# Kernel optimization log

Measured on AMD Instinct MI355X. Metric: run time of the kernel, lower is better.

The kernel has to match this reference:

```python
import jax, jax.numpy as jnp
import numpy as np

B, S, T, D = 4, 2, 1024, 512
H = 8
HD = D // H
EPS = 1e-6
LN_EPS = 1e-5


def setup_inputs() -> dict:
    key = jax.random.key(0)
    ks = jax.random.split(key, 12)
    def lin(k, fan_in, shape):
        bound = 1.0 / np.sqrt(fan_in)
        return jax.random.uniform(k, shape, jnp.float32, -bound, bound)
    return {
        "hidden_states": jax.random.normal(ks[0], (B, S, T, D), jnp.float32),
        "Wq": lin(ks[1], D, (D, D)), "bq": lin(ks[2], D, (D,)),
        "Wk": lin(ks[3], D, (D, D)), "bk": lin(ks[4], D, (D,)),
        "Wv": lin(ks[5], D, (D, D)), "bv": lin(ks[6], D, (D,)),
        "Wo": lin(ks[7], D, (D, D)), "bo": lin(ks[8], D, (D,)),
        "ln_g": jnp.ones((S, D), jnp.float32),
        "ln_b": jnp.zeros((S, D), jnp.float32),
        "gate_alpha": jnp.full((S,), 0.01, jnp.float32),
    }


def _heads(x):
    # [B,T,D] -> [B,H,T,HD]
    return x.reshape(B, T, H, HD).transpose(0, 2, 1, 3)


def _layernorm(x, g, b):
    mu = jnp.mean(x, axis=-1, keepdims=True)
    var = jnp.var(x, axis=-1, keepdims=True)
    return (x - mu) * jax.lax.rsqrt(var + LN_EPS) * g + b


def reference(hidden_states, Wq, bq, Wk, bk, Wv, bv, Wo, bo, ln_g, ln_b, gate_alpha):
    h1, h2 = hidden_states[:, 0], hidden_states[:, 1]  # [B,T,D]
    proj = lambda x, W, b: jnp.einsum('btd,ed->bte', x, W) + b
    Q1, K1, V1 = _heads(proj(h1, Wq, bq)), _heads(proj(h1, Wk, bk)), _heads(proj(h1, Wv, bv))
    Q2, K2, V2 = _heads(proj(h2, Wq, bq)), _heads(proj(h2, Wk, bk)), _heads(proj(h2, Wv, bv))
    scale = 1.0 / np.sqrt(HD)
    L12 = jnp.einsum('bhqd,bhkd->bhqk', Q1, K2) * scale
    L21 = jnp.einsum('bhqd,bhkd->bhqk', Q2, K1) * scale
    S12 = jax.nn.softmax(L12, axis=-1)
    S21 = jax.nn.softmax(L21, axis=-1)
    M = S12 + S21 + EPS
    A12 = S12 / M
    A21 = S21 / M
    H1 = jnp.einsum('bhqk,bhkd->bhqd', A12, V2).transpose(0, 2, 1, 3).reshape(B, T, D)
    H2 = jnp.einsum('bhqk,bhkd->bhqd', A21, V1).transpose(0, 2, 1, 3).reshape(B, T, D)
    H1 = _layernorm(jnp.einsum('btd,ed->bte', H1, Wo) + bo, ln_g[0], ln_b[0])
    H2 = _layernorm(jnp.einsum('btd,ed->bte', H2, Wo) + bo, ln_g[1], ln_b[1])
    attn = jnp.stack([H1, H2], axis=1)  # [B,2,T,D]
    return hidden_states + attn * gate_alpha[None, :, None, None]
```

## Files before the change

### kernel.cpp

```cpp
#include <hip/hip_runtime.h>

#define DEVI __device__ __forceinline__

typedef __bf16 v8bf __attribute__((ext_vector_type(8)));
typedef float  v4f  __attribute__((ext_vector_type(4)));
typedef short  v4s  __attribute__((ext_vector_type(4)));

DEVI unsigned short f2bf(float f) {
  unsigned u = __builtin_bit_cast(unsigned, f);
  u += 0x7fffu + ((u >> 16) & 1u);
  return (unsigned short)(u >> 16);
}
DEVI v4f MFMA32(v8bf a, v8bf b, v4f c) {
  return __builtin_amdgcn_mfma_f32_16x16x32_bf16(a, b, c, 0, 0, 0);
}
DEVI v8bf ldfrag(const unsigned short* p) {
  return __builtin_bit_cast(v8bf, *(const uint4*)p);
}
DEVI v4s ld4s(const unsigned short* p) {
  return __builtin_bit_cast(v4s, *(const uint2*)p);
}
DEVI unsigned pkbf(float lo, float hi) {
  unsigned a = __builtin_bit_cast(unsigned, hi) + 0x8000u;
  unsigned b = __builtin_bit_cast(unsigned, lo) + 0x8000u;
  return __builtin_amdgcn_perm(a, b, 0x07060302u);
}

#if __has_builtin(__builtin_amdgcn_mfma_f32_16x16x16bf16_1k)
#define HAVE_MFMA16 1
DEVI v4f MFMA16(v4s a, v4s b, v4f c) {
  return __builtin_amdgcn_mfma_f32_16x16x16bf16_1k(a, b, c, 0, 0, 0);
}
#else
#define HAVE_MFMA16 0
#endif

#if __has_builtin(__builtin_amdgcn_global_load_lds)
DEVI void g2l(const unsigned short* g, unsigned short* l) {
  __builtin_amdgcn_global_load_lds(
      (const __attribute__((address_space(1))) unsigned int*)g,
      (__attribute__((address_space(3))) unsigned int*)l, 16, 0, 0);
}
#else
DEVI void g2l(const unsigned short* g, unsigned short* l) {
  *(uint4*)((char*)l + (threadIdx.x & 63) * 16) = *(const uint4*)g;
}
#endif

__global__ __launch_bounds__(256) void convert_kernel(
    const float* __restrict__ X, const float* __restrict__ Wq,
    const float* __restrict__ Wk, const float* __restrict__ Wv,
    const float* __restrict__ Wo, unsigned short* __restrict__ dst)
{
  int t = blockIdx.x * 256 + threadIdx.x;
  int idx = t * 4;
  const float* src;
  if (idx < 4194304) {
    src = X + idx;
  } else {
    int u = idx - 4194304;
    int w = u >> 18;
    const float* W = (w == 0) ? Wq : (w == 1) ? Wk : (w == 2) ? Wv : Wo;
    src = W + (u & 262143);
  }
  float4 f = *(const float4*)src;
  uint2 o;
  o.x = pkbf(f.x, f.y);
  o.y = pkbf(f.z, f.w);
  *(uint2*)&dst[idx] = o;
}

template<int OUTM, int BM>
__global__ __launch_bounds__(256) void gemm_bt(
    const unsigned short* __restrict__ A,
    const unsigned short* __restrict__ W0, const unsigned short* __restrict__ W1,
    const unsigned short* __restrict__ W2,
    const float* __restrict__ b0, const float* __restrict__ b1, const float* __restrict__ b2,
    void* __restrict__ C0, void* __restrict__ C1, void* __restrict__ C2)
{
  const int K = 512, N = 512;
  const int MI = BM / 32;
  const int PER = (BM / 8 + 16) / 4;
  __shared__ unsigned short sAB[(BM + 128) * 64];
  const int z = blockIdx.z;
  const unsigned short* W = (z == 0) ? W0 : (z == 1) ? W1 : W2;
  const float* bias = (z == 0) ? b0 : (z == 1) ? b1 : b2;
  void* C = (z == 0) ? C0 : (z == 1) ? C1 : C2;

  const int tid = threadIdx.x;
  const int lane = tid & 63, wave = tid >> 6;
  const int l15 = lane & 15, quad = lane >> 4, swl = l15 & 7;
  const int lrow = lane >> 3;
  const int lc8 = ((lane & 7) ^ (lrow & 7)) * 8;
  const int wm = (wave >> 1) * (BM / 2), wn = (wave & 1) * 64;
  const int mbase = blockIdx.y * BM, nbase = blockIdx.x * 128;

  const unsigned short* gsrc[PER];
  unsigned short* ldst[PER];
#pragma unroll
  for (int t = 0; t < PER; t++) {
    int c = wave * PER + t;
    ldst[t] = &sAB[c * 512];
    if (c < BM / 8) gsrc[t] = A + (size_t)(mbase + c * 8 + lrow) * K + lc8;
    else            gsrc[t] = W + (size_t)(nbase + (c - BM / 8) * 8 + lrow) * K + lc8;
  }

  v4f acc[MI][4] = {};

  for (int kt = 0; kt < K; kt += 64) {
    __syncthreads();
#pragma unroll
    for (int t = 0; t < PER; t++) g2l(gsrc[t] + kt, ldst[t]);
    __syncthreads();
#pragma unroll
    for (int s = 0; s < 2; s++) {
      v8bf af[MI], bf[4];
#pragma unroll
      for (int i = 0; i < MI; i++)
        af[i] = ldfrag(&sAB[(wm + i * 16 + l15) * 64 + ((s * 4 + quad) ^ swl) * 8]);
#pragma unroll
      for (int j = 0; j < 4; j++)
        bf[j] = ldfrag(&sAB[(BM + wn + j * 16 + l15) * 64 + ((s * 4 + quad) ^ swl) * 8]);
#pragma unroll
      for (int i = 0; i < MI; i++)
#pragma unroll
        for (int j = 0; j < 4; j++)
          acc[i][j] = MFMA32(af[i], bf[j], acc[i][j]);
    }
  }

#pragma unroll
  for (int i = 0; i < MI; i++)
#pragma unroll
    for (int j = 0; j < 4; j++) {
      int row0 = mbase + wm + i * 16 + quad * 4;
      int col = nbase + wn + j * 16 + l15;
      float v[4];
#pragma unroll
      for (int r = 0; r < 4; r++) v[r] = acc[i][j][r] + bias[col];
      if (OUTM == 1) {
#pragma unroll
        for (int r = 0; r < 4; r++) ((float*)C)[(size_t)(row0 + r) * N + col] = v[r];
      } else if (z == 2) {
        int bs = row0 >> 10, t0 = row0 & 1023;
        int hh = col >> 6, hd = col & 63;
        uint2 o;
        o.x = pkbf(v[0], v[1]);
        o.y = pkbf(v[2], v[3]);
        *(uint2*)&((unsigned short*)C)[(size_t)((bs * 8 + hh) * 64 + hd) * 1024 + t0] = o;
      } else {
#pragma unroll
        for (int r = 0; r < 4; r++)
          ((unsigned short*)C)[(size_t)(row0 + r) * N + col] = f2bf(v[r]);
      }
    }
}

__global__ __launch_bounds__(512, 2) void attn_kernel(
    const unsigned short* __restrict__ Qg, const unsigned short* __restrict__ Kg,
    const unsigned short* __restrict__ VTg, unsigned short* __restrict__ Hc)
{
  __shared__ unsigned short sK[2][64][64];
  __shared__ unsigned short sV[2][64][64];
  __shared__ float sPf[8][16][68];
#if !HAVE_MFMA16
  __shared__ unsigned short sR[8][16][64];
#endif

  const int pair = blockIdx.x & 31;
  const int b = pair >> 3, h = pair & 7;
  const int qt = blockIdx.x >> 5;
  const int tid = threadIdx.x;
  const int lane = tid & 63, wave = tid >> 6;
  const int l15 = lane & 15, quad = lane >> 4, swl = l15 & 7;
  const int lrow = lane >> 3;
  const int lc8 = ((lane & 7) ^ (lrow & 7)) * 8;
  const int d = wave & 1, qg = wave >> 1;
  const int qbase = qt * 64 + qg * 16;
  const float scale = 0.125f;

  const unsigned short* kgp[2];
  const unsigned short* vgp[2];
#pragma unroll
  for (int st = 0; st < 2; st++) {
    kgp[st] = Kg + (size_t)((b * 2 + st) * 1024) * 512 + h * 64;
    vgp[st] = VTg + (size_t)(((b * 2 + st) * 8 + h) * 64) * 1024;
  }

  v8bf qf[2];
#pragma unroll
  for (int s = 0; s < 2; s++) {
    int qrow = (b * 2 + d) * 1024 + qbase + l15;
    qf[s] = ldfrag(&Qg[(size_t)qrow * 512 + h * 64 + s * 32 + quad * 8]);
  }

  unsigned short* lK = &sK[0][0][0];
  unsigned short* lV = &sV[0][0][0];

  float lacc = 0.f;
  {
    const unsigned short* gA[2];
    unsigned short* lA[2];
#pragma unroll
    for (int t = 0; t < 2; t++) {
      int c = wave * 2 + t;
      gA[t] = kgp[c >> 3] + (size_t)((c & 7) * 8 + lrow) * 512 + lc8;
      lA[t] = lK + c * 512;
    }
    for (int kt = 0; kt < 16; kt++) {
      __syncthreads();
#pragma unroll
      for (int t = 0; t < 2; t++) g2l(gA[t] + kt * 32768, lA[t]);
      __syncthreads();
      v4f acc[4] = {};
#pragma unroll
      for (int s = 0; s < 2; s++)
#pragma unroll
        for (int j = 0; j < 4; j++) {
          v8bf kf = ldfrag(&sK[1 - d][j * 16 + l15][((s * 4 + quad) ^ swl) * 8]);
          acc[j] = MFMA32(kf, qf[s], acc[j]);
        }
#pragma unroll
      for (int j = 0; j < 4; j++)
#pragma unroll
        for (int r = 0; r < 4; r++)
          lacc += __expf(acc[j][r] * scale);
    }
  }
  float v = lacc;
  v += __shfl_xor(v, 16);
  v += __shfl_xor(v, 32);
  const float ll = __logf(v);

  v4f oacc[4] = {};
  {
    const unsigned short* gB[4];
    unsigned short* lB[4];
    int stp[4];
#pragma unroll
    for (int t = 0; t < 4; t++) {
      int c = wave * 4 + t;
      if (c < 16) {
        gB[t] = kgp[c >> 3] + (size_t)((c & 7) * 8 + lrow) * 512 + lc8;
        stp[t] = 32768;
        lB[t] = lK + c * 512;
      } else {
        int cv = c - 16;
        gB[t] = vgp[cv >> 3] + (size_t)((cv & 7) * 8 + lrow) * 1024 + lc8;
        stp[t] = 64;
        lB[t] = lV + cv * 512;
      }
    }

    float* sp = &sPf[wave][l15][0];
    const float* spo = &sPf[wave ^ 1][l15][0];

    for (int kt = 0; kt < 16; kt++) {
      __syncthreads();
#pragma unroll
      for (int t = 0; t < 4; t++) g2l(gB[t] + kt * stp[t], lB[t]);
      __syncthreads();

      v4f acc[4] = {};
#pragma unroll
      for (int s = 0; s < 2; s++)
#pragma unroll
        for (int j = 0; j < 4; j++) {
          v8bf kf = ldfrag(&sK[1 - d][j * 16 + l15][((s * 4 + quad) ^ swl) * 8]);
          acc[j] = MFMA32(kf, qf[s], acc[j]);
        }

#pragma unroll
      for (int j = 0; j < 4; j++) {
        v4f p;
#pragma unroll
        for (int r = 0; r < 4; r++) p[r] = __expf(fmaf(acc[j][r], scale, -ll));
        *(v4f*)&sp[j * 16 + quad * 4] = p;
      }
      __syncthreads();

#pragma unroll
      for (int j = 0; j < 4; j++) {
        v4f ps = *(const v4f*)&sp[j * 16 + quad * 4];
        v4f po = *(const v4f*)&spo[j * 16 + quad * 4];
        float r0 = ps[0] * __builtin_amdgcn_rcpf(ps[0] + po[0] + 1e-6f);
        float r1 = ps[1] * __builtin_amdgcn_rcpf(ps[1] + po[1] + 1e-6f);
        float r2 = ps[2] * __builtin_amdgcn_rcpf(ps[2] + po[2] + 1e-6f);
        float r3 = ps[3] * __builtin_amdgcn_rcpf(ps[3] + po[3] + 1e-6f);
        uint2 w;
        w.x = pkbf(r0, r1);
        w.y = pkbf(r2, r3);
#if HAVE_MFMA16
        v4s af = __builtin_bit_cast(v4s, w);
#pragma unroll
        for (int nt = 0; nt < 4; nt++) {
          v4s vf = ld4s(&sV[1 - d][nt * 16 + l15]
                          [((j * 2 + (quad >> 1)) ^ swl) * 8 + (quad & 1) * 4]);
          oacc[nt] = MFMA16(af, vf, oacc[nt]);
        }
#else
        *(uint2*)&sR[wave][l15][((j * 2 + (quad >> 1)) ^ swl) * 8 + (quad & 1) * 4] = w;
#endif
      }
#if !HAVE_MFMA16
#pragma unroll
      for (int kh = 0; kh < 2; kh++) {
        v8bf afr = ldfrag(&sR[wave][l15][((kh * 4 + quad) ^ swl) * 8]);
#pragma unroll
        for (int nt = 0; nt < 4; nt++) {
          v8bf vf = ldfrag(&sV[1 - d][nt * 16 + l15][((kh * 4 + quad) ^ swl) * 8]);
          oacc[nt] = MFMA32(afr, vf, oacc[nt]);
        }
      }
#endif
    }
  }

#pragma unroll
  for (int nt = 0; nt < 4; nt++)
#pragma unroll
    for (int r = 0; r < 4; r++) {
      int row = (b * 2 + d) * 1024 + qbase + quad * 4 + r;
      int col = h * 64 + nt * 16 + l15;
      Hc[(size_t)row * 512 + col] = f2bf(oacc[nt][r]);
    }
}

__global__ __launch_bounds__(256) void ln_kernel(
    const float* __restrict__ P, const float* __restrict__ hidden,
    const float* __restrict__ ln_g, const float* __restrict__ ln_b,
    const float* __restrict__ gate, float* __restrict__ out)
{
  const int row = blockIdx.x;
  const int s = (row >> 10) & 1;
  const int tid = threadIdx.x;
  const int d0 = tid * 2;
  float2 x = *(const float2*)&P[(size_t)row * 512 + d0];
  float s1 = x.x + x.y;
  float s2 = x.x * x.x + x.y * x.y;
#pragma unroll
  for (int m = 1; m < 64; m <<= 1) { s1 += __shfl_xor(s1, m); s2 += __shfl_xor(s2, m); }
  __shared__ float r1[4], r2[4];
  if ((tid & 63) == 0) { r1[tid >> 6] = s1; r2[tid >> 6] = s2; }
  __syncthreads();
  s1 = r1[0] + r1[1] + r1[2] + r1[3];
  s2 = r2[0] + r2[1] + r2[2] + r2[3];
  float mu = s1 * (1.f / 512.f);
  float var = s2 * (1.f / 512.f) - mu * mu;
  float rs = rsqrtf(var + 1e-5f);
  float al = gate[s];
  float2 hv = *(const float2*)&hidden[(size_t)row * 512 + d0];
  float2 o;
  o.x = hv.x + ((x.x - mu) * rs * ln_g[s * 512 + d0]     + ln_b[s * 512 + d0])     * al;
  o.y = hv.y + ((x.y - mu) * rs * ln_g[s * 512 + d0 + 1] + ln_b[s * 512 + d0 + 1]) * al;
  *(float2*)&out[(size_t)row * 512 + d0] = o;
}

extern "C" void kernel_launch(void* const* d_in, const int* in_sizes, int n_in,
                              void* d_out, int out_size, void* d_ws, size_t ws_size,
                              hipStream_t stream)
{
  const float* hidden = (const float*)d_in[0];
  const float* Wq = (const float*)d_in[1];
  const float* bq = (const float*)d_in[2];
  const float* Wk = (const float*)d_in[3];
  const float* bk = (const float*)d_in[4];
  const float* Wv = (const float*)d_in[5];
  const float* bv = (const float*)d_in[6];
  const float* Wo = (const float*)d_in[7];
  const float* bo = (const float*)d_in[8];
  const float* ln_g = (const float*)d_in[9];
  const float* ln_b = (const float*)d_in[10];
  const float* gate = (const float*)d_in[11];

  unsigned short* U = (unsigned short*)d_ws;
  unsigned short* Xbf = U;
  unsigned short* Wqb = U + 4194304;
  unsigned short* Wkb = U + 4456448;
  unsigned short* Wvb = U + 4718592;
  unsigned short* Wob = U + 4980736;
  unsigned short* Qg  = U + 5242880;
  unsigned short* Kg  = U + 9437184;
  unsigned short* VT  = U + 13631488;
  unsigned short* Hc  = U + 17825792;
  float* P = (float*)((char*)d_ws + 44302336);

  convert_kernel<<<dim3(5120), 256, 0, stream>>>(hidden, Wq, Wk, Wv, Wo, Xbf);
  gemm_bt<0, 128><<<dim3(4, 64, 3), 256, 0, stream>>>(Xbf, Wqb, Wkb, Wvb, bq, bk, bv, Qg, Kg, VT);
  attn_kernel<<<dim3(512), 512, 0, stream>>>(Qg, Kg, VT, Hc);
  gemm_bt<1, 64><<<dim3(4, 128, 1), 256, 0, stream>>>(Hc, Wob, Wob, Wob, bo, bo, bo, P, P, P);
  ln_kernel<<<dim3(8192), 256, 0, stream>>>(P, hidden, ln_g, ln_b, gate, (float*)d_out);
}
```

Before: 203.1 us.

## Pair both directions per wave in attention, store Wo output bf16, wave-per-row LN

The attention kernel now has each wave compute both cross-attention directions for its 16 query rows. The pairwise normalisation S12/(S12+S21) is therefore done in registers, with no LDS round trip or extra block barrier per tile, and the block shrinks to 256 threads. The Wo projection writes bf16 instead of fp32, which halves that intermediate's traffic. The layernorm kernel processes one row per wave with vectorised loads and no shared-memory reduction. In exchange, registers per thread roughly double and the LN input loses precision to bf16 rounding.

```diff
diff --git a/kernel.cpp b/kernel.cpp
--- a/kernel.cpp
+++ b/kernel.cpp
@@ -25,6 +25,8 @@
   unsigned b = __builtin_bit_cast(unsigned, lo) + 0x8000u;
   return __builtin_amdgcn_perm(a, b, 0x07060302u);
 }
+DEVI float lo2f(unsigned u) { return __builtin_bit_cast(float, u << 16); }
+DEVI float hi2f(unsigned u) { return __builtin_bit_cast(float, u & 0xffff0000u); }
 
 #if __has_builtin(__builtin_amdgcn_mfma_f32_16x16x16bf16_1k)
 #define HAVE_MFMA16 1
@@ -156,16 +158,12 @@
     }
 }
 
-__global__ __launch_bounds__(512, 2) void attn_kernel(
+__global__ __launch_bounds__(256, 2) void attn_kernel(
     const unsigned short* __restrict__ Qg, const unsigned short* __restrict__ Kg,
     const unsigned short* __restrict__ VTg, unsigned short* __restrict__ Hc)
 {
   __shared__ unsigned short sK[2][64][64];
   __shared__ unsigned short sV[2][64][64];
-  __shared__ float sPf[8][16][68];
-#if !HAVE_MFMA16
-  __shared__ unsigned short sR[8][16][64];
-#endif
 
   const int pair = blockIdx.x & 31;
   const int b = pair >> 3, h = pair & 7;
@@ -175,8 +173,7 @@
   const int l15 = lane & 15, quad = lane >> 4, swl = l15 & 7;
   const int lrow = lane >> 3;
   const int lc8 = ((lane & 7) ^ (lrow & 7)) * 8;
-  const int d = wave & 1, qg = wave >> 1;
-  const int qbase = qt * 64 + qg * 16;
+  const int qbase = qt * 64 + wave * 16;
   const float scale = 0.125f;
 
   const unsigned short* kgp[2];
@@ -187,59 +184,69 @@
     vgp[st] = VTg + (size_t)(((b * 2 + st) * 8 + h) * 64) * 1024;
   }
 
-  v8bf qf[2];
-#pragma unroll
-  for (int s = 0; s < 2; s++) {
-    int qrow = (b * 2 + d) * 1024 + qbase + l15;
-    qf[s] = ldfrag(&Qg[(size_t)qrow * 512 + h * 64 + s * 32 + quad * 8]);
-  }
+  v8bf qf[2][2];
+#pragma unroll
+  for (int d = 0; d < 2; d++)
+#pragma unroll
+    for (int s = 0; s < 2; s++) {
+      int qrow = (b * 2 + d) * 1024 + qbase + l15;
+      qf[d][s] = ldfrag(&Qg[(size_t)qrow * 512 + h * 64 + s * 32 + quad * 8]);
+    }
 
   unsigned short* lK = &sK[0][0][0];
   unsigned short* lV = &sV[0][0][0];
 
-  float lacc = 0.f;
+  float lacc[2] = {0.f, 0.f};
   {
-    const unsigned short* gA[2];
-    unsigned short* lA[2];
-#pragma unroll
-    for (int t = 0; t < 2; t++) {
-      int c = wave * 2 + t;
+    const unsigned short* gA[4];
+    unsigned short* lA[4];
+#pragma unroll
+    for (int t = 0; t < 4; t++) {
+      int c = wave * 4 + t;
       gA[t] = kgp[c >> 3] + (size_t)((c & 7) * 8 + lrow) * 512 + lc8;
       lA[t] = lK + c * 512;
     }
     for (int kt = 0; kt < 16; kt++) {
       __syncthreads();
 #pragma unroll
-      for (int t = 0; t < 2; t++) g2l(gA[t] + kt * 32768, lA[t]);
+      for (int t = 0; t < 4; t++) g2l(gA[t] + kt * 32768, lA[t]);
       __syncthreads();
-      v4f acc[4] = {};
+      v4f acc[2][4] = {};
 #pragma unroll
       for (int s = 0; s < 2; s++)
 #pragma unroll
-        for (int j = 0; j < 4; j++) {
-          v8bf kf = ldfrag(&sK[1 - d][j * 16 + l15][((s * 4 + quad) ^ swl) * 8]);
-          acc[j] = MFMA32(kf, qf[s], acc[j]);
-        }
-#pragma unroll
-      for (int j = 0; j < 4; j++)
-#pragma unroll
-        for (int r = 0; r < 4; r++)
-          lacc += __expf(acc[j][r] * scale);
-    }
-  }
-  float v = lacc;
-  v += __shfl_xor(v, 16);
-  v += __shfl_xor(v, 32);
-  const float ll = __logf(v);
-
-  v4f oacc[4] = {};
+        for (int d = 0; d < 2; d++)
+#pragma unroll
+          for (int j = 0; j < 4; j++) {
+            v8bf kf = ldfrag(&sK[1 - d][j * 16 + l15][((s * 4 + quad) ^ swl) * 8]);
+            acc[d][j] = MFMA32(kf, qf[d][s], acc[d][j]);
+          }
+#pragma unroll
+      for (int d = 0; d < 2; d++)
+#pragma unroll
+        for (int j = 0; j < 4; j++)
+#pragma unroll
+          for (int r = 0; r < 4; r++)
+            lacc[d] += __expf(acc[d][j][r] * scale);
+    }
+  }
+  float ll[2];
+#pragma unroll
+  for (int d = 0; d < 2; d++) {
+    float v = lacc[d];
+    v += __shfl_xor(v, 16);
+    v += __shfl_xor(v, 32);
+    ll[d] = __logf(v);
+  }
+
+  v4f oacc[2][4] = {};
   {
-    const unsigned short* gB[4];
-    unsigned short* lB[4];
-    int stp[4];
-#pragma unroll
-    for (int t = 0; t < 4; t++) {
-      int c = wave * 4 + t;
+    const unsigned short* gB[8];
+    unsigned short* lB[8];
+    int stp[8];
+#pragma unroll
+    for (int t = 0; t < 8; t++) {
+      int c = wave * 8 + t;
       if (c < 16) {
         gB[t] = kgp[c >> 3] + (size_t)((c & 7) * 8 + lrow) * 512 + lc8;
         stp[t] = 32768;
@@ -252,108 +259,123 @@
       }
     }
 
-    float* sp = &sPf[wave][l15][0];
-    const float* spo = &sPf[wave ^ 1][l15][0];
-
     for (int kt = 0; kt < 16; kt++) {
       __syncthreads();
 #pragma unroll
-      for (int t = 0; t < 4; t++) g2l(gB[t] + kt * stp[t], lB[t]);
+      for (int t = 0; t < 8; t++) g2l(gB[t] + kt * stp[t], lB[t]);
       __syncthreads();
 
-      v4f acc[4] = {};
+      v4f acc[2][4] = {};
 #pragma unroll
       for (int s = 0; s < 2; s++)
 #pragma unroll
-        for (int j = 0; j < 4; j++) {
-          v8bf kf = ldfrag(&sK[1 - d][j * 16 + l15][((s * 4 + quad) ^ swl) * 8]);
-          acc[j] = MFMA32(kf, qf[s], acc[j]);
+        for (int d = 0; d < 2; d++)
+#pragma unroll
+          for (int j = 0; j < 4; j++) {
+            v8bf kf = ldfrag(&sK[1 - d][j * 16 + l15][((s * 4 + quad) ^ swl) * 8]);
+            acc[d][j] = MFMA32(kf, qf[d][s], acc[d][j]);
+          }
+
+#pragma unroll
+      for (int j = 0; j < 4; j++) {
+        float r0[4], r1[4];
+#pragma unroll
+        for (int r = 0; r < 4; r++) {
+          float p0 = __expf(fmaf(acc[0][j][r], scale, -ll[0]));
+          float p1 = __expf(fmaf(acc[1][j][r], scale, -ll[1]));
+          float ri = __builtin_amdgcn_rcpf(p0 + p1 + 1e-6f);
+          r0[r] = p0 * ri;
+          r1[r] = p1 * ri;
         }
-
-#pragma unroll
-      for (int j = 0; j < 4; j++) {
-        v4f p;
-#pragma unroll
-        for (int r = 0; r < 4; r++) p[r] = __expf(fmaf(acc[j][r], scale, -ll));
-        *(v4f*)&sp[j * 16 + quad * 4] = p;
-      }
-      __syncthreads();
-
-#pragma unroll
-      for (int j = 0; j < 4; j++) {
-        v4f ps = *(const v4f*)&sp[j * 16 + quad * 4];
-        v4f po = *(const v4f*)&spo[j * 16 + quad * 4];
-        float r0 = ps[0] * __builtin_amdgcn_rcpf(ps[0] + po[0] + 1e-6f);
-        float r1 = ps[1] * __builtin_amdgcn_rcpf(ps[1] + po[1] + 1e-6f);
-        float r2 = ps[2] * __builtin_amdgcn_rcpf(ps[2] + po[2] + 1e-6f);
-        float r3 = ps[3] * __builtin_amdgcn_rcpf(ps[3] + po[3] + 1e-6f);
-        uint2 w;
-        w.x = pkbf(r0, r1);
-        w.y = pkbf(r2, r3);
 #if HAVE_MFMA16
-        v4s af = __builtin_bit_cast(v4s, w);
+        uint2 w0, w1;
+        w0.x = pkbf(r0[0], r0[1]); w0.y = pkbf(r0[2], r0[3]);
+        w1.x = pkbf(r1[0], r1[1]); w1.y = pkbf(r1[2], r1[3]);
+        v4s af0 = __builtin_bit_cast(v4s, w0);
+        v4s af1 = __builtin_bit_cast(v4s, w1);
+        int vcol = ((j * 2 + (quad >> 1)) ^ swl) * 8 + (quad & 1) * 4;
 #pragma unroll
         for (int nt = 0; nt < 4; nt++) {
-          v4s vf = ld4s(&sV[1 - d][nt * 16 + l15]
-                          [((j * 2 + (quad >> 1)) ^ swl) * 8 + (quad & 1) * 4]);
-          oacc[nt] = MFMA16(af, vf, oacc[nt]);
+          v4s vf0 = ld4s(&sV[1][nt * 16 + l15][vcol]);
+          v4s vf1 = ld4s(&sV[0][nt * 16 + l15][vcol]);
+          oacc[0][nt] = MFMA16(af0, vf0, oacc[0][nt]);
+          oacc[1][nt] = MFMA16(af1, vf1, oacc[1][nt]);
         }
 #else
-        *(uint2*)&sR[wave][l15][((j * 2 + (quad >> 1)) ^ swl) * 8 + (quad & 1) * 4] = w;
+#pragma unroll
+        for (int d = 0; d < 2; d++) {
+          float (&cb)[4] = (d == 0) ? r0 : r1;
+          v8bf a;
+#pragma unroll
+          for (int jj = 0; jj < 8; jj++) {
+            int src = l15 + 16 * ((jj >> 2) + (quad & 1) * 2);
+            float v = __shfl(cb[jj & 3], src);
+            a[jj] = __builtin_bit_cast(__bf16, f2bf(v));
+          }
+#pragma unroll
+          for (int nt = 0; nt < 4; nt++) {
+            v8bf vf = ldfrag(&sV[1 - d][nt * 16 + l15]
+                               [(((j & 2) * 2 + quad) ^ swl) * 8]);
+            oacc[d][nt] = MFMA32(a, vf, oacc[d][nt]);
+          }
+        }
 #endif
       }
-#if !HAVE_MFMA16
-#pragma unroll
-      for (int kh = 0; kh < 2; kh++) {
-        v8bf afr = ldfrag(&sR[wave][l15][((kh * 4 + quad) ^ swl) * 8]);
-#pragma unroll
-        for (int nt = 0; nt < 4; nt++) {
-          v8bf vf = ldfrag(&sV[1 - d][nt * 16 + l15][((kh * 4 + quad) ^ swl) * 8]);
-          oacc[nt] = MFMA32(afr, vf, oacc[nt]);
-        }
+    }
+  }
+
+#pragma unroll
+  for (int d = 0; d < 2; d++)
+#pragma unroll
+    for (int nt = 0; nt < 4; nt++)
+#pragma unroll
+      for (int r = 0; r < 4; r++) {
+        int row = (b * 2 + d) * 1024 + qbase + quad * 4 + r;
+        int col = h * 64 + nt * 16 + l15;
+        Hc[(size_t)row * 512 + col] = f2bf(oacc[d][nt][r]);
       }
-#endif
-    }
-  }
-
-#pragma unroll
-  for (int nt = 0; nt < 4; nt++)
-#pragma unroll
-    for (int r = 0; r < 4; r++) {
-      int row = (b * 2 + d) * 1024 + qbase + quad * 4 + r;
-      int col = h * 64 + nt * 16 + l15;
-      Hc[(size_t)row * 512 + col] = f2bf(oacc[nt][r]);
-    }
 }
 
 __global__ __launch_bounds__(256) void ln_kernel(
-    const float* __restrict__ P, const float* __restrict__ hidden,
+    const unsigned short* __restrict__ Pb, const float* __restrict__ hidden,
     const float* __restrict__ ln_g, const float* __restrict__ ln_b,
     const float* __restrict__ gate, float* __restrict__ out)
 {
-  const int row = blockIdx.x;
+  const int row = blockIdx.x * 4 + (threadIdx.x >> 6);
   const int s = (row >> 10) & 1;
-  const int tid = threadIdx.x;
-  const int d0 = tid * 2;
-  float2 x = *(const float2*)&P[(size_t)row * 512 + d0];
-  float s1 = x.x + x.y;
-  float s2 = x.x * x.x + x.y * x.y;
+  const int lane = threadIdx.x & 63;
+  const int d0 = lane * 8;
+
+  uint4 up = *(const uint4*)&Pb[(size_t)row * 512 + d0];
+  float x[8] = { lo2f(up.x), hi2f(up.x), lo2f(up.y), hi2f(up.y),
+                 lo2f(up.z), hi2f(up.z), lo2f(up.w), hi2f(up.w) };
+  float s1 = 0.f, s2 = 0.f;
+#pragma unroll
+  for (int i = 0; i < 8; i++) { s1 += x[i]; s2 += x[i] * x[i]; }
 #pragma unroll
   for (int m = 1; m < 64; m <<= 1) { s1 += __shfl_xor(s1, m); s2 += __shfl_xor(s2, m); }
-  __shared__ float r1[4], r2[4];
-  if ((tid & 63) == 0) { r1[tid >> 6] = s1; r2[tid >> 6] = s2; }
-  __syncthreads();
-  s1 = r1[0] + r1[1] + r1[2] + r1[3];
-  s2 = r2[0] + r2[1] + r2[2] + r2[3];
   float mu = s1 * (1.f / 512.f);
   float var = s2 * (1.f / 512.f) - mu * mu;
   float rs = rsqrtf(var + 1e-5f);
   float al = gate[s];
-  float2 hv = *(const float2*)&hidden[(size_t)row * 512 + d0];
-  float2 o;
-  o.x = hv.x + ((x.x - mu) * rs * ln_g[s * 512 + d0]     + ln_b[s * 512 + d0])     * al;
-  o.y = hv.y + ((x.y - mu) * rs * ln_g[s * 512 + d0 + 1] + ln_b[s * 512 + d0 + 1]) * al;
-  *(float2*)&out[(size_t)row * 512 + d0] = o;
+
+  float4 h0 = *(const float4*)&hidden[(size_t)row * 512 + d0];
+  float4 h1 = *(const float4*)&hidden[(size_t)row * 512 + d0 + 4];
+  float4 g0 = *(const float4*)&ln_g[s * 512 + d0];
+  float4 g1 = *(const float4*)&ln_g[s * 512 + d0 + 4];
+  float4 bb0 = *(const float4*)&ln_b[s * 512 + d0];
+  float4 bb1 = *(const float4*)&ln_b[s * 512 + d0 + 4];
+  float4 o0, o1;
+  o0.x = h0.x + ((x[0] - mu) * rs * g0.x + bb0.x) * al;
+  o0.y = h0.y + ((x[1] - mu) * rs * g0.y + bb0.y) * al;
+  o0.z = h0.z + ((x[2] - mu) * rs * g0.z + bb0.z) * al;
+  o0.w = h0.w + ((x[3] - mu) * rs * g0.w + bb0.w) * al;
+  o1.x = h1.x + ((x[4] - mu) * rs * g1.x + bb1.x) * al;
+  o1.y = h1.y + ((x[5] - mu) * rs * g1.y + bb1.y) * al;
+  o1.z = h1.z + ((x[6] - mu) * rs * g1.z + bb1.z) * al;
+  o1.w = h1.w + ((x[7] - mu) * rs * g1.w + bb1.w) * al;
+  *(float4*)&out[(size_t)row * 512 + d0] = o0;
+  *(float4*)&out[(size_t)row * 512 + d0 + 4] = o1;
 }
 
 extern "C" void kernel_launch(void* const* d_in, const int* in_sizes, int n_in,
@@ -383,11 +405,11 @@
   unsigned short* Kg  = U + 9437184;
   unsigned short* VT  = U + 13631488;
   unsigned short* Hc  = U + 17825792;
-  float* P = (float*)((char*)d_ws + 44302336);
+  unsigned short* Pb  = (unsigned short*)((char*)d_ws + 44302336);
 
   convert_kernel<<<dim3(5120), 256, 0, stream>>>(hidden, Wq, Wk, Wv, Wo, Xbf);
   gemm_bt<0, 128><<<dim3(4, 64, 3), 256, 0, stream>>>(Xbf, Wqb, Wkb, Wvb, bq, bk, bv, Qg, Kg, VT);
-  attn_kernel<<<dim3(512), 512, 0, stream>>>(Qg, Kg, VT, Hc);
-  gemm_bt<1, 64><<<dim3(4, 128, 1), 256, 0, stream>>>(Hc, Wob, Wob, Wob, bo, bo, bo, P, P, P);
-  ln_kernel<<<dim3(8192), 256, 0, stream>>>(P, hidden, ln_g, ln_b, gate, (float*)d_out);
-}
+  attn_kernel<<<dim3(512), 256, 0, stream>>>(Qg, Kg, VT, Hc);
+  gemm_bt<0, 64><<<dim3(4, 128, 1), 256, 0, stream>>>(Hc, Wob, Wob, Wob, bo, bo, bo, Pb, Pb, Pb);
+  ln_kernel<<<dim3(2048), 256, 0, stream>>>(Pb, hidden, ln_g, ln_b, gate, (float*)d_out);
+}
```

After: 190.3 us. -6.3%, faster.
